# Kernel optimization log

Hardware: AMD Instinct MI355X
Metric: run time of the kernel (lower is better)

## Reference

```python
import jax, jax.numpy as jnp
import numpy as np

TEMPERATURE = 8.0  # sqrt(d_k=64)
NEG_FILL = -1000.0


def setup_inputs() -> dict:
    key = jax.random.key(0)
    k1, k2, k3, k4 = jax.random.split(key, 4)
    B, Lq, Lk, D = 16, 2048, 2048, 64
    q = jax.random.normal(k1, (B, Lq, D), dtype=jnp.float32)
    k = jax.random.normal(k2, (B, Lk, D), dtype=jnp.float32)
    v = jax.random.normal(k3, (B, Lk, D), dtype=jnp.float32)
    pad_mask = jax.random.randint(k4, (B, Lk), 0, 2).astype(bool)
    return {"q": q, "k": k, "v": v, "pad_mask": pad_mask}


def reference(q, k, v, pad_mask):
    # scores: [B, Lq, Lk]
    attn = jnp.einsum('bqd,bkd->bqk', q, k) / TEMPERATURE
    # mask padded keys (broadcast over query dim, like pad_mask.unsqueeze(1))
    attn = jnp.where(pad_mask[:, None, :], NEG_FILL, attn)
    attn = jax.nn.softmax(attn, axis=-1)
    # dropout is identity in eval / p=0
    output = jnp.einsum('bqk,bkd->bqd', attn, v)
    return output, attn
```

## Files before the change

kernel.cpp:

```cpp
#include <hip/hip_runtime.h>
#include <hip/hip_bf16.h>

#define BB 16
#define LL 2048
#define DD 64

typedef __attribute__((ext_vector_type(8))) short short8t;
typedef __attribute__((ext_vector_type(4))) float f32x4;
typedef __attribute__((ext_vector_type(4))) unsigned short ushort4t;

__device__ __forceinline__ unsigned short f2bf(float x) {
  union { float f; unsigned int u; } c; c.f = x;
  unsigned int u = c.u;
  u += 0x7fffu + ((u >> 16) & 1u);
  return (unsigned short)(u >> 16);
}

__global__ void cvt_bf16(const float* __restrict__ in, unsigned short* __restrict__ out) {
  int i = (blockIdx.x * 256 + threadIdx.x) * 4;
  float4 v = *(const float4*)(in + i);
  ushort4t o;
  o.x = f2bf(v.x); o.y = f2bf(v.y); o.z = f2bf(v.z); o.w = f2bf(v.w);
  *(ushort4t*)(out + i) = o;
}

__global__ void vtrans(const float* __restrict__ v, unsigned short* __restrict__ vt) {
  __shared__ unsigned short t[64][66];
  int b = blockIdx.x >> 5, j0 = (blockIdx.x & 31) * 64;
  const float* src = v + ((size_t)b * LL + j0) * DD;
#pragma unroll
  for (int i = 0; i < 16; ++i) {
    int lin = i * 256 + threadIdx.x;
    int j = lin >> 6, d = lin & 63;
    t[j][d] = f2bf(src[lin]);
  }
  __syncthreads();
  unsigned short* dst = vt + (size_t)b * DD * LL;
#pragma unroll
  for (int i = 0; i < 16; ++i) {
    int lin = i * 256 + threadIdx.x;
    int d = lin >> 6, j = lin & 63;
    dst[(size_t)d * LL + j0 + j] = t[j][d];
  }
}

__device__ __forceinline__ void async_cp16(const unsigned short* src, unsigned short* dst_lds) {
  __builtin_amdgcn_global_load_lds(
      (const __attribute__((address_space(1))) unsigned int*)src,
      (__attribute__((address_space(3))) unsigned int*)dst_lds, 16, 0, 0);
}

__global__ void __launch_bounds__(256, 2)
attn_main(const unsigned short* __restrict__ Qb, const unsigned short* __restrict__ Kb,
          const unsigned short* __restrict__ VTb, const int* __restrict__ mask,
          float* __restrict__ out, float* __restrict__ attn) {
  __shared__ __align__(16) unsigned short TB[4][3][2048];
  __shared__ float redL[4][64];
  __shared__ float rinvL[64];

  const int tid = threadIdx.x;
  const int w = tid >> 6;
  const int l = tid & 63;
  const int l15 = l & 15;
  const int g = l >> 4;

  const int b = blockIdx.x >> 5;
  const int q0 = (blockIdx.x & 31) << 6;

  unsigned short* KB = &TB[w][0][0];
  unsigned short* VB = &TB[w][1][0];
  unsigned short* PB = &TB[w][2][0];

  const unsigned short* Kbb = Kb + (size_t)b * LL * DD;
  const unsigned short* VTbb = VTb + (size_t)b * DD * LL;
  const int* maskb = mask + b * LL;

  short8t qf[4][2];
  {
    const unsigned short* qbase = Qb + ((size_t)b * LL + q0 + l15) * DD + 8 * g;
#pragma unroll
    for (int mi = 0; mi < 4; ++mi)
#pragma unroll
      for (int h = 0; h < 2; ++h)
        qf[mi][h] = *(const short8t*)(qbase + mi * 16 * DD + 32 * h);
  }

  float ls[4][4];
#pragma unroll
  for (int mi = 0; mi < 4; ++mi)
#pragma unroll
    for (int r = 0; r < 4; ++r) ls[mi][r] = 0.f;

  for (int t = w; t < 64; t += 4) {
    const int k0 = t * 32;
    {
      const unsigned short* gs = Kbb + (size_t)k0 * DD;
#pragma unroll
      for (int i = 0; i < 4; ++i) {
        int row = i * 8 + (l >> 3);
        int ce = (l & 7) * 8;
        async_cp16(gs + row * 64 + (ce ^ ((row & 3) << 4)), KB + i * 512);
      }
    }
    int mk0 = maskb[k0 + l15];
    int mk1 = maskb[k0 + 16 + l15];
    asm volatile("s_waitcnt vmcnt(0)" ::: "memory");

    f32x4 sacc[4][2] = {};
    short8t kf[2][2];
#pragma unroll
    for (int ni = 0; ni < 2; ++ni)
#pragma unroll
      for (int h = 0; h < 2; ++h) {
        int row = 16 * ni + l15;
        int col = (32 * h + 8 * g) ^ ((l15 & 3) << 4);
        kf[ni][h] = *(const short8t*)(KB + row * 64 + col);
      }
#pragma unroll
    for (int mi = 0; mi < 4; ++mi)
#pragma unroll
      for (int ni = 0; ni < 2; ++ni)
#pragma unroll
        for (int h = 0; h < 2; ++h)
          sacc[mi][ni] = __builtin_amdgcn_mfma_f32_16x16x32_bf16(qf[mi][h], kf[ni][h], sacc[mi][ni], 0, 0, 0);

#pragma unroll
    for (int mi = 0; mi < 4; ++mi)
#pragma unroll
      for (int ni = 0; ni < 2; ++ni) {
        int mk = ni ? mk1 : mk0;
#pragma unroll
        for (int r = 0; r < 4; ++r) {
          float sv = mk ? -1000.f : sacc[mi][ni][r] * 0.125f;
          ls[mi][r] += __expf(sv);
        }
      }
  }

#pragma unroll
  for (int mi = 0; mi < 4; ++mi)
#pragma unroll
    for (int r = 0; r < 4; ++r) {
      float s = ls[mi][r];
      s += __shfl_xor(s, 1);
      s += __shfl_xor(s, 2);
      s += __shfl_xor(s, 4);
      s += __shfl_xor(s, 8);
      if (l15 == 0) redL[w][16 * mi + 4 * g + r] = s;
    }
  __syncthreads();
  if (tid < 64)
    rinvL[tid] = 1.0f / (redL[0][tid] + redL[1][tid] + redL[2][tid] + redL[3][tid]);
  __syncthreads();

  float rinv_[4][4];
#pragma unroll
  for (int mi = 0; mi < 4; ++mi)
#pragma unroll
    for (int r = 0; r < 4; ++r) rinv_[mi][r] = rinvL[16 * mi + 4 * g + r];

  f32x4 oacc[4][4] = {};
  for (int t = w; t < 64; t += 4) {
    const int k0 = t * 32;
    {
      const unsigned short* gs = Kbb + (size_t)k0 * DD;
#pragma unroll
      for (int i = 0; i < 4; ++i) {
        int row = i * 8 + (l >> 3);
        int ce = (l & 7) * 8;
        async_cp16(gs + row * 64 + (ce ^ ((row & 3) << 4)), KB + i * 512);
      }
    }
    {
      const unsigned short* gs = VTbb + k0;
#pragma unroll
      for (int i = 0; i < 4; ++i) {
        int row = i * 16 + (l >> 2);
        int ce = (l & 3) * 8;
        async_cp16(gs + (size_t)row * LL + (ce ^ ((row & 1) << 4)), VB + i * 512);
      }
    }
    int mk0 = maskb[k0 + l15];
    int mk1 = maskb[k0 + 16 + l15];
    asm volatile("s_waitcnt vmcnt(0)" ::: "memory");

    f32x4 sacc[4][2] = {};
    short8t kf[2][2];
#pragma unroll
    for (int ni = 0; ni < 2; ++ni)
#pragma unroll
      for (int h = 0; h < 2; ++h) {
        int row = 16 * ni + l15;
        int col = (32 * h + 8 * g) ^ ((l15 & 3) << 4);
        kf[ni][h] = *(const short8t*)(KB + row * 64 + col);
      }
#pragma unroll
    for (int mi = 0; mi < 4; ++mi)
#pragma unroll
      for (int ni = 0; ni < 2; ++ni)
#pragma unroll
        for (int h = 0; h < 2; ++h)
          sacc[mi][ni] = __builtin_amdgcn_mfma_f32_16x16x32_bf16(qf[mi][h], kf[ni][h], sacc[mi][ni], 0, 0, 0);

#pragma unroll
    for (int mi = 0; mi < 4; ++mi)
#pragma unroll
      for (int ni = 0; ni < 2; ++ni) {
        int mk = ni ? mk1 : mk0;
#pragma unroll
        for (int r = 0; r < 4; ++r) {
          float sv = mk ? -1000.f : sacc[mi][ni][r] * 0.125f;
          float p = __expf(sv) * rinv_[mi][r];
          int qloc = 16 * mi + 4 * g + r;
          attn[((size_t)(b * LL + q0 + qloc)) * LL + k0 + 16 * ni + l15] = p;
          PB[qloc * 32 + ((16 * ni + l15) ^ ((r & 1) << 4))] = f2bf(p);
        }
      }

    short8t pf[4], vf[4];
#pragma unroll
    for (int mi = 0; mi < 4; ++mi)
      pf[mi] = *(const short8t*)(PB + (16 * mi + l15) * 32 + ((8 * g) ^ ((l & 1) << 4)));
#pragma unroll
    for (int ni = 0; ni < 4; ++ni)
      vf[ni] = *(const short8t*)(VB + (16 * ni + l15) * 32 + ((8 * g) ^ ((l & 1) << 4)));
#pragma unroll
    for (int mi = 0; mi < 4; ++mi)
#pragma unroll
      for (int ni = 0; ni < 4; ++ni)
        oacc[mi][ni] = __builtin_amdgcn_mfma_f32_16x16x32_bf16(pf[mi], vf[ni], oacc[mi][ni], 0, 0, 0);
  }

  __syncthreads();
  float* OB = (float*)&TB[0][0][0];
  if (w) {
#pragma unroll
    for (int mi = 0; mi < 4; ++mi)
#pragma unroll
      for (int ni = 0; ni < 4; ++ni)
#pragma unroll
        for (int r = 0; r < 4; ++r)
          OB[(w - 1) * 4096 + (16 * mi + 4 * g + r) * 64 + 16 * ni + l15] = oacc[mi][ni][r];
  }
  __syncthreads();
  if (w == 0) {
#pragma unroll
    for (int mi = 0; mi < 4; ++mi)
#pragma unroll
      for (int ni = 0; ni < 4; ++ni)
#pragma unroll
        for (int r = 0; r < 4; ++r) {
          int pos = (16 * mi + 4 * g + r) * 64 + 16 * ni + l15;
          float o = oacc[mi][ni][r] + OB[pos] + OB[4096 + pos] + OB[8192 + pos];
          out[((size_t)(b * LL + q0 + 16 * mi + 4 * g + r)) * DD + 16 * ni + l15] = o;
        }
  }
}

extern "C" void kernel_launch(void* const* d_in, const int* in_sizes, int n_in,
                              void* d_out, int out_size, void* d_ws, size_t ws_size,
                              hipStream_t stream) {
  const float* q = (const float*)d_in[0];
  const float* k = (const float*)d_in[1];
  const float* v = (const float*)d_in[2];
  const int* pm = (const int*)d_in[3];

  float* out = (float*)d_out;
  float* attn = out + (size_t)BB * LL * DD;

  unsigned short* Qb = (unsigned short*)d_ws;
  unsigned short* Kb = Qb + (size_t)BB * LL * DD;
  unsigned short* VT = Kb + (size_t)BB * LL * DD;

  cvt_bf16<<<2048, 256, 0, stream>>>(q, Qb);
  cvt_bf16<<<2048, 256, 0, stream>>>(k, Kb);
  vtrans<<<512, 256, 0, stream>>>(v, VT);
  attn_main<<<512, 256, 0, stream>>>(Qb, Kb, VT, pm, out, attn);
}
```

Baseline: 100.3 us.

## Double-buffer K and prefetch V/mask across iterations, use nontemporal attn stores

Both passes now use two per-wave K buffers in LDS and issue the async loads for the next key tile (plus its mask values and, in the second pass, the V tile) before doing the current tile's MFMA and softmax work. The intent is to hide global-load latency that was previously exposed by a full vmcnt(0) wait each iteration. The large attention-matrix writes become nontemporal stores to reduce cache pollution, and masked scores skip the exponential by writing zero directly. LDS per block grows to hold the extra buffer, and correctness relies on a hand-tuned vmcnt(32) count that assumes the number of outstanding store operations.

```diff
diff --git a/kernel.cpp b/kernel.cpp
--- a/kernel.cpp
+++ b/kernel.cpp
@@ -54,7 +54,7 @@
 attn_main(const unsigned short* __restrict__ Qb, const unsigned short* __restrict__ Kb,
           const unsigned short* __restrict__ VTb, const int* __restrict__ mask,
           float* __restrict__ out, float* __restrict__ attn) {
-  __shared__ __align__(16) unsigned short TB[4][3][2048];
+  __shared__ __align__(16) unsigned short TB[4][8192];
   __shared__ float redL[4][64];
   __shared__ float rinvL[64];
 
@@ -67,14 +67,34 @@
   const int b = blockIdx.x >> 5;
   const int q0 = (blockIdx.x & 31) << 6;
 
-  unsigned short* KB = &TB[w][0][0];
-  unsigned short* VB = &TB[w][1][0];
-  unsigned short* PB = &TB[w][2][0];
+  unsigned short* K0 = &TB[w][0];
+  unsigned short* K1 = &TB[w][2048];
+  unsigned short* VB = &TB[w][4096];
+  unsigned short* PB = &TB[w][6144];
 
   const unsigned short* Kbb = Kb + (size_t)b * LL * DD;
   const unsigned short* VTbb = VTb + (size_t)b * DD * LL;
   const int* maskb = mask + b * LL;
 
+  auto loadK = [&](int k0, unsigned short* KB) {
+    const unsigned short* gs = Kbb + (size_t)k0 * DD;
+#pragma unroll
+    for (int i2 = 0; i2 < 4; ++i2) {
+      int row = i2 * 8 + (l >> 3);
+      int ce = (l & 7) * 8;
+      async_cp16(gs + row * 64 + (ce ^ ((row & 3) << 4)), KB + i2 * 512);
+    }
+  };
+  auto loadV = [&](int k0) {
+    const unsigned short* gs = VTbb + k0;
+#pragma unroll
+    for (int i2 = 0; i2 < 4; ++i2) {
+      int row = i2 * 16 + (l >> 2);
+      int ce = (l & 3) * 8;
+      async_cp16(gs + (size_t)row * LL + (ce ^ ((row & 1) << 4)), VB + i2 * 512);
+    }
+  };
+
   short8t qf[4][2];
   {
     const unsigned short* qbase = Qb + ((size_t)b * LL + q0 + l15) * DD + 8 * g;
@@ -91,22 +111,9 @@
 #pragma unroll
     for (int r = 0; r < 4; ++r) ls[mi][r] = 0.f;
 
-  for (int t = w; t < 64; t += 4) {
-    const int k0 = t * 32;
-    {
-      const unsigned short* gs = Kbb + (size_t)k0 * DD;
-#pragma unroll
-      for (int i = 0; i < 4; ++i) {
-        int row = i * 8 + (l >> 3);
-        int ce = (l & 7) * 8;
-        async_cp16(gs + row * 64 + (ce ^ ((row & 3) << 4)), KB + i * 512);
-      }
-    }
-    int mk0 = maskb[k0 + l15];
-    int mk1 = maskb[k0 + 16 + l15];
+  auto stepA = [&](int t, int tn, unsigned short* KBc, unsigned short* KBn,
+                   int mk0c, int mk1c, int& mk0n, int& mk1n) {
     asm volatile("s_waitcnt vmcnt(0)" ::: "memory");
-
-    f32x4 sacc[4][2] = {};
     short8t kf[2][2];
 #pragma unroll
     for (int ni = 0; ni < 2; ++ni)
@@ -114,8 +121,13 @@
       for (int h = 0; h < 2; ++h) {
         int row = 16 * ni + l15;
         int col = (32 * h + 8 * g) ^ ((l15 & 3) << 4);
-        kf[ni][h] = *(const short8t*)(KB + row * 64 + col);
+        kf[ni][h] = *(const short8t*)(KBc + row * 64 + col);
       }
+    loadK(tn * 32, KBn);
+    mk0n = maskb[tn * 32 + l15];
+    mk1n = maskb[tn * 32 + 16 + l15];
+
+    f32x4 sacc[4][2] = {};
 #pragma unroll
     for (int mi = 0; mi < 4; ++mi)
 #pragma unroll
@@ -123,18 +135,30 @@
 #pragma unroll
         for (int h = 0; h < 2; ++h)
           sacc[mi][ni] = __builtin_amdgcn_mfma_f32_16x16x32_bf16(qf[mi][h], kf[ni][h], sacc[mi][ni], 0, 0, 0);
-
 #pragma unroll
     for (int mi = 0; mi < 4; ++mi)
 #pragma unroll
       for (int ni = 0; ni < 2; ++ni) {
-        int mk = ni ? mk1 : mk0;
+        int mk = ni ? mk1c : mk0c;
 #pragma unroll
         for (int r = 0; r < 4; ++r) {
-          float sv = mk ? -1000.f : sacc[mi][ni][r] * 0.125f;
-          ls[mi][r] += __expf(sv);
+          float p = mk ? 0.f : __expf(sacc[mi][ni][r] * 0.125f);
+          ls[mi][r] += p;
         }
       }
+  };
+
+  {
+    loadK(w * 32, K0);
+    int a0 = maskb[w * 32 + l15], a1 = maskb[w * 32 + 16 + l15];
+    int b0, b1;
+    for (int j = 0; j < 8; ++j) {
+      int t = w + 8 * j;
+      stepA(t, t + 4, K0, K1, a0, a1, b0, b1);
+      int t2 = t + 4;
+      int tn = (j == 7) ? w : (t2 + 4);
+      stepA(t2, tn, K1, K0, b0, b1, a0, a1);
+    }
   }
 
 #pragma unroll
@@ -160,40 +184,31 @@
     for (int r = 0; r < 4; ++r) rinv_[mi][r] = rinvL[16 * mi + 4 * g + r];
 
   f32x4 oacc[4][4] = {};
-  for (int t = w; t < 64; t += 4) {
+  auto stepB = [&](int t, int tn, unsigned short* KBc, unsigned short* KBn,
+                   int mk0c, int mk1c, int& mk0n, int& mk1n) {
+    asm volatile("s_waitcnt vmcnt(32)" ::: "memory");
     const int k0 = t * 32;
-    {
-      const unsigned short* gs = Kbb + (size_t)k0 * DD;
-#pragma unroll
-      for (int i = 0; i < 4; ++i) {
-        int row = i * 8 + (l >> 3);
-        int ce = (l & 7) * 8;
-        async_cp16(gs + row * 64 + (ce ^ ((row & 3) << 4)), KB + i * 512);
-      }
-    }
-    {
-      const unsigned short* gs = VTbb + k0;
-#pragma unroll
-      for (int i = 0; i < 4; ++i) {
-        int row = i * 16 + (l >> 2);
-        int ce = (l & 3) * 8;
-        async_cp16(gs + (size_t)row * LL + (ce ^ ((row & 1) << 4)), VB + i * 512);
-      }
-    }
-    int mk0 = maskb[k0 + l15];
-    int mk1 = maskb[k0 + 16 + l15];
-    asm volatile("s_waitcnt vmcnt(0)" ::: "memory");
-
-    f32x4 sacc[4][2] = {};
-    short8t kf[2][2];
+    short8t kf[2][2], vf[4];
 #pragma unroll
     for (int ni = 0; ni < 2; ++ni)
 #pragma unroll
       for (int h = 0; h < 2; ++h) {
         int row = 16 * ni + l15;
         int col = (32 * h + 8 * g) ^ ((l15 & 3) << 4);
-        kf[ni][h] = *(const short8t*)(KB + row * 64 + col);
+        kf[ni][h] = *(const short8t*)(KBc + row * 64 + col);
       }
+#pragma unroll
+    for (int ni = 0; ni < 4; ++ni)
+      vf[ni] = *(const short8t*)(VB + (16 * ni + l15) * 32 + ((8 * g) ^ ((l & 1) << 4)));
+    asm volatile("s_waitcnt lgkmcnt(0)" ::: "memory");
+    __builtin_amdgcn_sched_barrier(0);
+
+    loadK(tn * 32, KBn);
+    mk0n = maskb[tn * 32 + l15];
+    mk1n = maskb[tn * 32 + 16 + l15];
+    loadV(tn * 32);
+
+    f32x4 sacc[4][2] = {};
 #pragma unroll
     for (int mi = 0; mi < 4; ++mi)
 #pragma unroll
@@ -206,33 +221,46 @@
     for (int mi = 0; mi < 4; ++mi)
 #pragma unroll
       for (int ni = 0; ni < 2; ++ni) {
-        int mk = ni ? mk1 : mk0;
+        int mk = ni ? mk1c : mk0c;
 #pragma unroll
         for (int r = 0; r < 4; ++r) {
-          float sv = mk ? -1000.f : sacc[mi][ni][r] * 0.125f;
-          float p = __expf(sv) * rinv_[mi][r];
+          float p = mk ? 0.f : __expf(sacc[mi][ni][r] * 0.125f) * rinv_[mi][r];
           int qloc = 16 * mi + 4 * g + r;
-          attn[((size_t)(b * LL + q0 + qloc)) * LL + k0 + 16 * ni + l15] = p;
+          __builtin_nontemporal_store(p, &attn[((size_t)(b * LL + q0 + qloc)) * LL + k0 + 16 * ni + l15]);
           PB[qloc * 32 + ((16 * ni + l15) ^ ((r & 1) << 4))] = f2bf(p);
         }
       }
 
-    short8t pf[4], vf[4];
+    short8t pf[4];
 #pragma unroll
     for (int mi = 0; mi < 4; ++mi)
       pf[mi] = *(const short8t*)(PB + (16 * mi + l15) * 32 + ((8 * g) ^ ((l & 1) << 4)));
-#pragma unroll
-    for (int ni = 0; ni < 4; ++ni)
-      vf[ni] = *(const short8t*)(VB + (16 * ni + l15) * 32 + ((8 * g) ^ ((l & 1) << 4)));
 #pragma unroll
     for (int mi = 0; mi < 4; ++mi)
 #pragma unroll
       for (int ni = 0; ni < 4; ++ni)
         oacc[mi][ni] = __builtin_amdgcn_mfma_f32_16x16x32_bf16(pf[mi], vf[ni], oacc[mi][ni], 0, 0, 0);
-  }
-
-  __syncthreads();
-  float* OB = (float*)&TB[0][0][0];
+  };
+
+  {
+    loadK(w * 32, K0);
+    int a0 = maskb[w * 32 + l15], a1 = maskb[w * 32 + 16 + l15];
+    loadV(w * 32);
+    asm volatile("s_waitcnt vmcnt(0)" ::: "memory");
+    int b0, b1;
+    for (int j = 0; j < 8; ++j) {
+      int t = w + 8 * j;
+      stepB(t, t + 4, K0, K1, a0, a1, b0, b1);
+      int t2 = t + 4;
+      int tn = (j == 7) ? w : (t2 + 4);
+      stepB(t2, tn, K1, K0, b0, b1, a0, a1);
+    }
+  }
+
+  asm volatile("s_waitcnt vmcnt(0)" ::: "memory");
+
+  __syncthreads();
+  float* OB = (float*)&TB[0][0];
   if (w) {
 #pragma unroll
     for (int mi = 0; mi < 4; ++mi)
```

Result: slower. 116.4 us (+16.1%).
